# Optimization experiments

Hardware: AMD Instinct MI355X
Metric: run time of the kernel (lower is better)

## Reference

```python
import jax, jax.numpy as jnp
import numpy as np

B, S, D_MODEL, D_K = 4, 4096, 1024, 128
NEG = jnp.float32(-1e30)  # acts as -inf for masking; exp underflows to exactly 0 in fp32


def setup_inputs() -> dict:
    key = jax.random.key(0)
    ks = jax.random.split(key, 8)
    sc = 1.0 / np.sqrt(D_MODEL)
    x = jax.random.normal(ks[0], (B, S, D_MODEL), jnp.float32)
    padding_mask = (jax.random.uniform(ks[1], (B, S)) > 0.05).astype(jnp.float32)
    Wq = jax.random.normal(ks[2], (D_MODEL, D_K), jnp.float32) * sc
    bq = jax.random.normal(ks[3], (D_K,), jnp.float32) * 0.01
    Wk = jax.random.normal(ks[4], (D_MODEL, D_K), jnp.float32) * sc
    bk = jax.random.normal(ks[5], (D_K,), jnp.float32) * 0.01
    Wv = jax.random.normal(ks[6], (D_MODEL, D_K), jnp.float32) * sc
    bv = jax.random.normal(ks[7], (D_K,), jnp.float32) * 0.01
    return {"x": x, "padding_mask": padding_mask, "Wq": Wq, "bq": bq,
            "Wk": Wk, "bk": bk, "Wv": Wv, "bv": bv}


def reference(x, padding_mask, Wq, bq, Wk, bk, Wv, bv):
    # Self-attention path (enc_dec_layer_input is None), masked=True (causal).
    scale = jnp.sqrt(jnp.float32(Wq.shape[-1]))
    Q = x @ Wq + bq  # [B,S,Dk]
    K = x @ Wk + bk
    V = x @ Wv + bv
    scores = jnp.einsum('bqd,bkd->bqk', Q, K) / scale  # [B,S,S]
    # causal mask (torch: triu(1) filled with -inf) AND padding outer-product mask
    causal = jnp.tril(jnp.ones((S, S), dtype=bool))  # True = allowed
    pm = (padding_mask[:, :, None] * padding_mask[:, None, :]) > 0  # [B,S,S]
    allowed = causal[None] & pm
    scores = jnp.where(allowed, scores, NEG)
    attn = jax.nn.softmax(scores, axis=-1)
    # torch: fully-masked query rows give NaN -> nan_to_num -> 0.
    # A query row is dead iff its own token is padded (diagonal is causally allowed).
    row_alive = padding_mask > 0  # [B,S]
    attn = jnp.where(row_alive[:, :, None], attn, 0.0)
    out = jnp.einsum('bqk,bkd->bqd', attn, V)  # [B,S,Dk]
    return out
```

## Files before the change

kernel.cpp:

```cpp
#include <hip/hip_runtime.h>
#include <hip/hip_bf16.h>
#include <cstdint>

typedef __bf16 bf16x8 __attribute__((ext_vector_type(8)));
typedef float f32x4 __attribute__((ext_vector_type(4)));

#define MFMA16(a, b, c) __builtin_amdgcn_mfma_f32_16x16x32_bf16((a), (b), (c), 0, 0, 0)

__device__ __forceinline__ unsigned short f2bf(float f) {
  union { float f; unsigned u; } v; v.f = f;
  unsigned u = v.u;
  u += 0x7fffu + ((u >> 16) & 1u);
  return (unsigned short)(u >> 16);
}
__device__ __forceinline__ unsigned pk2(float a, float b) {
  __hip_bfloat162 h = __float22bfloat162_rn(make_float2(a, b));
  union { __hip_bfloat162 h; unsigned u; } v; v.h = h; return v.u;
}

__global__ __launch_bounds__(256) void convert_w(
    const float* __restrict__ Wq, const float* __restrict__ Wk,
    const float* __restrict__ Wv, unsigned short* __restrict__ wt) {
  int idx = blockIdx.x * 256 + threadIdx.x;
  int m = idx >> 17;
  int rem = idx & 131071;
  int k = rem >> 7;
  int n = rem & 127;
  const float* W = (m == 0) ? Wq : (m == 1) ? Wk : Wv;
  wt[(size_t)m * 131072 + (size_t)n * 1024 + k] = f2bf(W[(size_t)k * 128 + n]);
}

__global__ __launch_bounds__(256) void qkv_gemm(
    const float* __restrict__ x, const unsigned short* __restrict__ wt_all,
    const float* __restrict__ bq, const float* __restrict__ bk,
    const float* __restrict__ bv,
    unsigned short* __restrict__ Qg, unsigned short* __restrict__ Kg,
    unsigned short* __restrict__ Vtg) {
  __shared__ unsigned short x_lds[64][40];
  __shared__ unsigned short w_lds[128][40];
  const int tid = threadIdx.x;
  const int lane = tid & 63;
  const int w = tid >> 6;
  const int mode = blockIdx.y;
  const int m0 = blockIdx.x * 64;
  const unsigned short* wt = wt_all + (size_t)mode * 131072;
  const float* bias = (mode == 0) ? bq : (mode == 1) ? bk : bv;

  const int wr = (w >> 1) * 32;
  const int wc = (w & 1) * 64;
  const int lr = lane & 15;
  const int lk = (lane >> 4) * 8;

  f32x4 acc[2][4];
#pragma unroll
  for (int m = 0; m < 2; ++m)
#pragma unroll
    for (int n = 0; n < 4; ++n) acc[m][n] = (f32x4){0.f, 0.f, 0.f, 0.f};

  const int xr = tid >> 2;
  const int xc = (tid & 3) * 8;
  const int srow = tid >> 1;
  const int shalf = (tid & 1) * 16;
  const float* xrow = x + (size_t)(m0 + xr) * 1024 + xc;
  const unsigned short* wrow = wt + (size_t)srow * 1024 + shalf;

  float4 xa, xb; uint4 wv0, wv1;
  {
    const float4* s4 = (const float4*)xrow;
    xa = s4[0]; xb = s4[1];
    const uint4* ws4 = (const uint4*)wrow;
    wv0 = ws4[0]; wv1 = ws4[1];
  }

  for (int k0 = 0; k0 < 1024; k0 += 32) {
    __syncthreads();
    {
      uint4 xw;
      xw.x = pk2(xa.x, xa.y);  xw.y = pk2(xa.z, xa.w);
      xw.z = pk2(xb.x, xb.y);  xw.w = pk2(xb.z, xb.w);
      *(uint4*)&x_lds[xr][xc] = xw;
      *(uint4*)&w_lds[srow][shalf] = wv0;
      *(uint4*)&w_lds[srow][shalf + 8] = wv1;
    }
    __syncthreads();
    if (k0 + 32 < 1024) {
      const float4* s4 = (const float4*)(xrow + k0 + 32);
      xa = s4[0]; xb = s4[1];
      const uint4* ws4 = (const uint4*)(wrow + k0 + 32);
      wv0 = ws4[0]; wv1 = ws4[1];
    }
    bf16x8 af[2], bfr[4];
#pragma unroll
    for (int m = 0; m < 2; ++m) af[m] = *(const bf16x8*)&x_lds[wr + m * 16 + lr][lk];
#pragma unroll
    for (int n = 0; n < 4; ++n) bfr[n] = *(const bf16x8*)&w_lds[wc + n * 16 + lr][lk];
#pragma unroll
    for (int m = 0; m < 2; ++m)
#pragma unroll
      for (int n = 0; n < 4; ++n) acc[m][n] = MFMA16(af[m], bfr[n], acc[m][n]);
  }

  float bcol[4];
#pragma unroll
  for (int n = 0; n < 4; ++n) bcol[n] = bias[wc + n * 16 + lr];
#pragma unroll
  for (int m = 0; m < 2; ++m)
#pragma unroll
    for (int n = 0; n < 4; ++n)
#pragma unroll
      for (int r = 0; r < 4; ++r) {
        int grow = m0 + wr + m * 16 + (lane >> 4) * 4 + r;
        int col = wc + n * 16 + lr;
        float val = acc[m][n][r] + bcol[n];
        if (mode == 0) {
          val *= 0.08838834764831845f;
          Qg[(size_t)grow * 128 + col] = f2bf(val);
        } else if (mode == 1) {
          Kg[(size_t)grow * 128 + col] = f2bf(val);
        } else {
          int bb = grow >> 12, s = grow & 4095;
          Vtg[((size_t)bb * 128 + col) * 4096 + s] = f2bf(val);
        }
      }
}

struct AttnLds {
  union {
    unsigned short K_lds[64][136];
    unsigned short P_lds[4][16][68];
  } u;
  unsigned short V_lds[128][72];
};

__device__ __forceinline__ void attn_tiles(
    AttnLds& S, const unsigned short* __restrict__ Kb,
    const unsigned short* __restrict__ Vb, const float* __restrict__ pmb,
    int q0, int tstart, int tend,
    const bf16x8 (&qf)[4], float& mrow, float& lsum, f32x4 (&o)[8]) {
  const int tid = threadIdx.x;
  const int lane = tid & 63;
  const int w = tid >> 6;
  const int lr = lane & 15;
  const int lg = lane >> 4;
  const int lk = lg * 8;
  const int q_own = q0 + w * 16 + lr;

  for (int t = tstart; t < tend; ++t) {
    const int k0 = t * 64;
    __syncthreads();
    {
      int kr = tid >> 2, seg = (tid & 3) * 32;
      const uint4* src = (const uint4*)(Kb + (size_t)(k0 + kr) * 128 + seg);
      uint4 v0 = src[0], v1 = src[1], v2 = src[2], v3 = src[3];
      uint4* dst = (uint4*)&S.u.K_lds[kr][seg];
      dst[0] = v0; dst[1] = v1; dst[2] = v2; dst[3] = v3;
      int d = tid >> 1, half = (tid & 1) * 32;
      const uint4* vs = (const uint4*)(Vb + (size_t)d * 4096 + k0 + half);
      uint4 u0 = vs[0], u1 = vs[1], u2 = vs[2], u3 = vs[3];
      uint4* vdst = (uint4*)&S.V_lds[d][half];
      vdst[0] = u0; vdst[1] = u1; vdst[2] = u2; vdst[3] = u3;
    }
    __syncthreads();

    f32x4 st[4];
#pragma unroll
    for (int f = 0; f < 4; ++f) {
      st[f] = (f32x4){0.f, 0.f, 0.f, 0.f};
#pragma unroll
      for (int dc = 0; dc < 4; ++dc) {
        bf16x8 kf = *(const bf16x8*)&S.u.K_lds[f * 16 + lr][dc * 32 + lk];
        st[f] = MFMA16(kf, qf[dc], st[f]);
      }
    }

    const unsigned long long mb = __ballot(pmb[k0 + lane] > 0.f);
    unsigned nib[4];
#pragma unroll
    for (int f = 0; f < 4; ++f) nib[f] = (unsigned)(mb >> (16 * f + 4 * lg)) & 0xFu;

    __syncthreads();

    float mx = -1e30f;
    if (k0 + 63 > q0 + (w << 4)) {
#pragma unroll
      for (int f = 0; f < 4; ++f)
#pragma unroll
        for (int r = 0; r < 4; ++r) {
          const bool ok = (((nib[f] >> r) & 1u) != 0u) &&
                          (k0 + 16 * f + 4 * lg + r <= q_own);
          const float s = ok ? st[f][r] : -1e30f;
          st[f][r] = s;
          mx = fmaxf(mx, s);
        }
    } else {
#pragma unroll
      for (int f = 0; f < 4; ++f)
#pragma unroll
        for (int r = 0; r < 4; ++r) {
          const bool ok = ((nib[f] >> r) & 1u) != 0u;
          const float s = ok ? st[f][r] : -1e30f;
          st[f][r] = s;
          mx = fmaxf(mx, s);
        }
    }
    mx = fmaxf(mx, __shfl_xor(mx, 16));
    mx = fmaxf(mx, __shfl_xor(mx, 32));
    const float mnew = fmaxf(mrow, mx);
    const float alpha = __expf(mrow - mnew);
    mrow = mnew;

    float sum = 0.f;
#pragma unroll
    for (int f = 0; f < 4; ++f) {
      const float p0 = (st[f][0] < -1e29f) ? 0.f : __expf(st[f][0] - mnew);
      const float p1 = (st[f][1] < -1e29f) ? 0.f : __expf(st[f][1] - mnew);
      const float p2 = (st[f][2] < -1e29f) ? 0.f : __expf(st[f][2] - mnew);
      const float p3 = (st[f][3] < -1e29f) ? 0.f : __expf(st[f][3] - mnew);
      sum += (p0 + p1) + (p2 + p3);
      uint2 u; u.x = pk2(p0, p1); u.y = pk2(p2, p3);
      *(uint2*)&S.u.P_lds[w][lr][16 * f + 4 * lg] = u;
    }
    sum += __shfl_xor(sum, 16);
    sum += __shfl_xor(sum, 32);
    lsum = lsum * alpha + sum;
#pragma unroll
    for (int n = 0; n < 8; ++n) o[n] *= alpha;

    __asm__ volatile("s_waitcnt lgkmcnt(0)" ::: "memory");
#pragma unroll
    for (int kc = 0; kc < 2; ++kc) {
      bf16x8 pa = *(const bf16x8*)&S.u.P_lds[w][lr][kc * 32 + lk];
#pragma unroll
      for (int n = 0; n < 8; ++n) {
        bf16x8 vf = *(const bf16x8*)&S.V_lds[n * 16 + lr][kc * 32 + lk];
        o[n] = MFMA16(vf, pa, o[n]);
      }
    }
  }
}

__global__ __launch_bounds__(256, 4) void attn_fwd(
    const unsigned short* __restrict__ Qg, const unsigned short* __restrict__ Kg,
    const unsigned short* __restrict__ Vtg, const float* __restrict__ pmask,
    float* __restrict__ out) {
  __shared__ AttnLds S;
  const int tid = threadIdx.x;
  const int lane = tid & 63;
  const int w = tid >> 6;
  const int b = blockIdx.y;
  const int q0 = blockIdx.x * 64;
  const int lr = lane & 15;
  const int lg = lane >> 4;
  const int lk = lg * 8;

  bf16x8 qf[4];
  {
    const unsigned short* qp = Qg + ((size_t)b * 4096 + q0 + w * 16 + lr) * 128;
#pragma unroll
    for (int dc = 0; dc < 4; ++dc) qf[dc] = *(const bf16x8*)(qp + dc * 32 + lk);
  }
  float mrow = -1e30f, lsum = 0.f;
  f32x4 o[8];
#pragma unroll
  for (int n = 0; n < 8; ++n) o[n] = (f32x4){0.f, 0.f, 0.f, 0.f};

  attn_tiles(S, Kg + (size_t)b * 4096 * 128, Vtg + (size_t)b * 128 * 4096,
             pmask + (size_t)b * 4096, q0, 0, (q0 >> 6) + 1, qf, mrow, lsum, o);

  const int qrow = q0 + w * 16 + lr;
  const bool alive = pmask[(size_t)b * 4096 + qrow] > 0.f;
  const float inv = (alive && lsum > 0.f) ? 1.f / lsum : 0.f;
  float* op = out + ((size_t)b * 4096 + qrow) * 128 + 4 * lg;
#pragma unroll
  for (int n = 0; n < 8; ++n) {
    f32x4 v = o[n] * inv;
    *(f32x4*)(op + n * 16) = v;
  }
}

__global__ __launch_bounds__(256, 4) void attn_split(
    const unsigned short* __restrict__ Qg, const unsigned short* __restrict__ Kg,
    const unsigned short* __restrict__ Vtg, const float* __restrict__ pmask,
    float* __restrict__ out, unsigned short* __restrict__ o_part,
    float* __restrict__ ml_part) {
  __shared__ AttnLds S;
  const int tid = threadIdx.x;
  const int lane = tid & 63;
  const int w = tid >> 6;
  const int L = blockIdx.x;
  const int xcd = L & 7;
  const int b = xcd >> 1;
  const int s = ((L >> 3) << 1) | (xcd & 1);
  int qb, c, nch;
  if (s < 8) {
    qb = s; c = 0; nch = 1;
  } else {
    int g = 1;
#pragma unroll
    for (int gg = 2; gg <= 7; ++gg)
      if (s >= 4 * gg * (gg + 1)) g = gg;
    const int rel = s - 4 * g * (g + 1);
    const int qq = rel / (g + 1);
    qb = 8 * g + qq;
    c = rel - qq * (g + 1);
    nch = g + 1;
  }
  const int q0 = qb * 64;
  const int tstart = c * 8;
  const int tend = min(c * 8 + 8, qb + 1);
  const int lr = lane & 15;
  const int lg = lane >> 4;
  const int lk = lg * 8;

  bf16x8 qf[4];
  {
    const unsigned short* qp = Qg + ((size_t)b * 4096 + q0 + w * 16 + lr) * 128;
#pragma unroll
    for (int dc = 0; dc < 4; ++dc) qf[dc] = *(const bf16x8*)(qp + dc * 32 + lk);
  }
  float mrow = -1e30f, lsum = 0.f;
  f32x4 o[8];
#pragma unroll
  for (int n = 0; n < 8; ++n) o[n] = (f32x4){0.f, 0.f, 0.f, 0.f};

  attn_tiles(S, Kg + (size_t)b * 4096 * 128, Vtg + (size_t)b * 128 * 4096,
             pmask + (size_t)b * 4096, q0, tstart, tend, qf, mrow, lsum, o);

  if (nch == 1) {
    const int qrow = q0 + w * 16 + lr;
    const bool alive = pmask[(size_t)b * 4096 + qrow] > 0.f;
    const float inv = (alive && lsum > 0.f) ? 1.f / lsum : 0.f;
    float* op = out + ((size_t)b * 4096 + qrow) * 128 + 4 * lg;
#pragma unroll
    for (int n = 0; n < 8; ++n) {
      f32x4 v = o[n] * inv;
      *(f32x4*)(op + n * 16) = v;
    }
  } else {
    const int slot = b * 280 + (s - 8);
    unsigned short* op = o_part + ((size_t)slot * 64 + w * 16 + lr) * 128 + 4 * lg;
#pragma unroll
    for (int n = 0; n < 8; ++n) {
      uint2 u; u.x = pk2(o[n][0], o[n][1]); u.y = pk2(o[n][2], o[n][3]);
      *(uint2*)(op + n * 16) = u;
    }
    if (lane < 16) {
      float* mp = ml_part + ((size_t)slot * 64 + w * 16 + lane) * 2;
      mp[0] = mrow;
      mp[1] = lsum;
    }
  }
}

__global__ __launch_bounds__(256) void attn_combine(
    const unsigned short* __restrict__ o_part, const float* __restrict__ ml_part,
    const float* __restrict__ pmask, float* __restrict__ out) {
  const int tid = threadIdx.x;
  const int lane = tid & 63;
  const int w = tid >> 6;
  const int g = blockIdx.x * 4 + w;
  const int b = g / 3584;
  const int rem = g % 3584;
  const int qb = 8 + (rem >> 6);
  const int row = rem & 63;
  const int qrow = qb * 64 + row;
  const int grp = qb >> 3;
  const int nch = grp + 1;
  const int pbase = b * 280 + 4 * grp * (grp + 1) - 8 + (qb - 8 * grp) * nch;

  float m[8], l[8];
  float M = -1e30f;
#pragma unroll
  for (int c = 0; c < 8; ++c)
    if (c < nch) {
      const float* mp = ml_part + ((size_t)(pbase + c) * 64 + row) * 2;
      m[c] = mp[0];
      l[c] = mp[1];
      M = fmaxf(M, m[c]);
    }
  float L = 0.f, wgt[8];
#pragma unroll
  for (int c = 0; c < 8; ++c)
    if (c < nch) {
      wgt[c] = __expf(m[c] - M);
      L += wgt[c] * l[c];
    }
  float2 acc = {0.f, 0.f};
#pragma unroll
  for (int c = 0; c < 8; ++c)
    if (c < nch) {
      const unsigned u = *(const unsigned*)(o_part + ((size_t)(pbase + c) * 64 + row) * 128 + lane * 2);
      acc.x += wgt[c] * __uint_as_float(u << 16);
      acc.y += wgt[c] * __uint_as_float(u & 0xffff0000u);
    }
  const bool alive = pmask[(size_t)b * 4096 + qrow] > 0.f;
  const float inv = (alive && L > 0.f) ? 1.f / L : 0.f;
  float2* op = (float2*)(out + ((size_t)b * 4096 + qrow) * 128);
  op[lane] = make_float2(acc.x * inv, acc.y * inv);
}

extern "C" void kernel_launch(void* const* d_in, const int* in_sizes, int n_in,
                              void* d_out, int out_size, void* d_ws, size_t ws_size,
                              hipStream_t stream) {
  (void)in_sizes; (void)n_in; (void)out_size;
  const float* x  = (const float*)d_in[0];
  const float* pm = (const float*)d_in[1];
  const float* Wq = (const float*)d_in[2];
  const float* bq = (const float*)d_in[3];
  const float* Wk = (const float*)d_in[4];
  const float* bk = (const float*)d_in[5];
  const float* Wv = (const float*)d_in[6];
  const float* bv = (const float*)d_in[7];
  float* out = (float*)d_out;

  unsigned short* ws  = (unsigned short*)d_ws;
  unsigned short* wt  = ws;
  unsigned short* Qg  = ws + 393216;
  unsigned short* Kg  = Qg + 2097152;
  unsigned short* Vtg = Kg + 2097152;
  unsigned short* o_part = ws + 6684672;
  float* ml_part = (float*)(ws + 15859712);
  const size_t WS_NEED = 15859712u * 2u + 573440u;

  convert_w<<<1536, 256, 0, stream>>>(Wq, Wk, Wv, wt);
  qkv_gemm<<<dim3(256, 3), 256, 0, stream>>>(x, wt, bq, bk, bv, Qg, Kg, Vtg);
  if (ws_size >= WS_NEED) {
    attn_split<<<1152, 256, 0, stream>>>(Qg, Kg, Vtg, pm, out, o_part, ml_part);
    attn_combine<<<3584, 256, 0, stream>>>(o_part, ml_part, pm, out);
  } else {
    attn_fwd<<<dim3(64, 4), 256, 0, stream>>>(Qg, Kg, Vtg, pm, out);
  }
}
```

Before: 104.4 us.

## Fuse Q/K/V projections into one GEMM kernel sharing the x tile

Replaces the three-way grid split (one block per mode) with a single block computing Q, K and V for its 64-row slab. Each x tile is loaded from global and converted to bf16 once instead of three times. Global loads are double-buffered two k-steps ahead. In exchange, the grid shrinks from 768 to 256 blocks, each thread holds three times the accumulators, and more registers are live, which can lower occupancy and parallelism.

```diff
diff --git a/kernel.cpp b/kernel.cpp
--- a/kernel.cpp
+++ b/kernel.cpp
@@ -30,98 +30,138 @@
   wt[(size_t)m * 131072 + (size_t)n * 1024 + k] = f2bf(W[(size_t)k * 128 + n]);
 }
 
-__global__ __launch_bounds__(256) void qkv_gemm(
+__global__ __launch_bounds__(256) void qkv_fused(
     const float* __restrict__ x, const unsigned short* __restrict__ wt_all,
     const float* __restrict__ bq, const float* __restrict__ bk,
     const float* __restrict__ bv,
     unsigned short* __restrict__ Qg, unsigned short* __restrict__ Kg,
     unsigned short* __restrict__ Vtg) {
   __shared__ unsigned short x_lds[64][40];
-  __shared__ unsigned short w_lds[128][40];
+  __shared__ unsigned short w_lds[3][128][40];
   const int tid = threadIdx.x;
   const int lane = tid & 63;
   const int w = tid >> 6;
-  const int mode = blockIdx.y;
   const int m0 = blockIdx.x * 64;
-  const unsigned short* wt = wt_all + (size_t)mode * 131072;
-  const float* bias = (mode == 0) ? bq : (mode == 1) ? bk : bv;
-
   const int wr = (w >> 1) * 32;
   const int wc = (w & 1) * 64;
   const int lr = lane & 15;
   const int lk = (lane >> 4) * 8;
 
-  f32x4 acc[2][4];
-#pragma unroll
-  for (int m = 0; m < 2; ++m)
-#pragma unroll
-    for (int n = 0; n < 4; ++n) acc[m][n] = (f32x4){0.f, 0.f, 0.f, 0.f};
+  f32x4 acc[3][2][4];
+#pragma unroll
+  for (int md = 0; md < 3; ++md)
+#pragma unroll
+    for (int m = 0; m < 2; ++m)
+#pragma unroll
+      for (int n = 0; n < 4; ++n) acc[md][m][n] = (f32x4){0.f, 0.f, 0.f, 0.f};
 
   const int xr = tid >> 2;
   const int xc = (tid & 3) * 8;
   const int srow = tid >> 1;
   const int shalf = (tid & 1) * 16;
-  const float* xrow = x + (size_t)(m0 + xr) * 1024 + xc;
-  const unsigned short* wrow = wt + (size_t)srow * 1024 + shalf;
-
-  float4 xa, xb; uint4 wv0, wv1;
+  const float* xbase = x + (size_t)(m0 + xr) * 1024 + xc;
+  const unsigned short* w0p = wt_all + (size_t)srow * 1024 + shalf;
+  const unsigned short* w1p = w0p + 131072;
+  const unsigned short* w2p = w1p + 131072;
+
+  float4 xA0, xA1, xB0, xB1;
+  uint4 a0, a1, a2, a3, a4, a5, b0, b1, b2, b3, b4, b5;
   {
-    const float4* s4 = (const float4*)xrow;
-    xa = s4[0]; xb = s4[1];
-    const uint4* ws4 = (const uint4*)wrow;
-    wv0 = ws4[0]; wv1 = ws4[1];
-  }
-
-  for (int k0 = 0; k0 < 1024; k0 += 32) {
-    __syncthreads();
-    {
-      uint4 xw;
-      xw.x = pk2(xa.x, xa.y);  xw.y = pk2(xa.z, xa.w);
-      xw.z = pk2(xb.x, xb.y);  xw.w = pk2(xb.z, xb.w);
-      *(uint4*)&x_lds[xr][xc] = xw;
-      *(uint4*)&w_lds[srow][shalf] = wv0;
-      *(uint4*)&w_lds[srow][shalf + 8] = wv1;
-    }
-    __syncthreads();
-    if (k0 + 32 < 1024) {
-      const float4* s4 = (const float4*)(xrow + k0 + 32);
-      xa = s4[0]; xb = s4[1];
-      const uint4* ws4 = (const uint4*)(wrow + k0 + 32);
-      wv0 = ws4[0]; wv1 = ws4[1];
-    }
-    bf16x8 af[2], bfr[4];
-#pragma unroll
-    for (int m = 0; m < 2; ++m) af[m] = *(const bf16x8*)&x_lds[wr + m * 16 + lr][lk];
-#pragma unroll
-    for (int n = 0; n < 4; ++n) bfr[n] = *(const bf16x8*)&w_lds[wc + n * 16 + lr][lk];
+    const float4* p = (const float4*)xbase;
+    xA0 = p[0]; xA1 = p[1];
+    const uint4* q0 = (const uint4*)w0p; a0 = q0[0]; a1 = q0[1];
+    const uint4* q1 = (const uint4*)w1p; a2 = q1[0]; a3 = q1[1];
+    const uint4* q2 = (const uint4*)w2p; a4 = q2[0]; a5 = q2[1];
+  }
+  {
+    const float4* p = (const float4*)(xbase + 32);
+    xB0 = p[0]; xB1 = p[1];
+    const uint4* q0 = (const uint4*)(w0p + 32); b0 = q0[0]; b1 = q0[1];
+    const uint4* q1 = (const uint4*)(w1p + 32); b2 = q1[0]; b3 = q1[1];
+    const uint4* q2 = (const uint4*)(w2p + 32); b4 = q2[0]; b5 = q2[1];
+  }
+
+#define QKV_STORE(X0, X1, W0, W1, W2, W3, W4, W5)             \
+  {                                                            \
+    uint4 xw;                                                  \
+    xw.x = pk2(X0.x, X0.y); xw.y = pk2(X0.z, X0.w);            \
+    xw.z = pk2(X1.x, X1.y); xw.w = pk2(X1.z, X1.w);            \
+    *(uint4*)&x_lds[xr][xc] = xw;                              \
+    *(uint4*)&w_lds[0][srow][shalf] = W0;                      \
+    *(uint4*)&w_lds[0][srow][shalf + 8] = W1;                  \
+    *(uint4*)&w_lds[1][srow][shalf] = W2;                      \
+    *(uint4*)&w_lds[1][srow][shalf + 8] = W3;                  \
+    *(uint4*)&w_lds[2][srow][shalf] = W4;                      \
+    *(uint4*)&w_lds[2][srow][shalf + 8] = W5;                  \
+  }
+
+#define QKV_COMPUTE()                                          \
+  {                                                            \
+    bf16x8 af0 = *(const bf16x8*)&x_lds[wr + lr][lk];          \
+    bf16x8 af1 = *(const bf16x8*)&x_lds[wr + 16 + lr][lk];     \
+    _Pragma("unroll")                                          \
+    for (int md = 0; md < 3; ++md)                             \
+      _Pragma("unroll")                                        \
+      for (int n = 0; n < 4; ++n) {                            \
+        bf16x8 bfv = *(const bf16x8*)&w_lds[md][wc + n * 16 + lr][lk]; \
+        acc[md][0][n] = MFMA16(af0, bfv, acc[md][0][n]);       \
+        acc[md][1][n] = MFMA16(af1, bfv, acc[md][1][n]);       \
+      }                                                        \
+  }
+
+  for (int k0 = 0; k0 < 1024; k0 += 64) {
+    __syncthreads();
+    QKV_STORE(xA0, xA1, a0, a1, a2, a3, a4, a5);
+    __syncthreads();
+    if (k0 + 64 < 1024) {
+      const float4* p = (const float4*)(xbase + k0 + 64);
+      xA0 = p[0]; xA1 = p[1];
+      const uint4* q0 = (const uint4*)(w0p + k0 + 64); a0 = q0[0]; a1 = q0[1];
+      const uint4* q1 = (const uint4*)(w1p + k0 + 64); a2 = q1[0]; a3 = q1[1];
+      const uint4* q2 = (const uint4*)(w2p + k0 + 64); a4 = q2[0]; a5 = q2[1];
+    }
+    QKV_COMPUTE();
+    __syncthreads();
+    QKV_STORE(xB0, xB1, b0, b1, b2, b3, b4, b5);
+    __syncthreads();
+    if (k0 + 96 < 1024) {
+      const float4* p = (const float4*)(xbase + k0 + 96);
+      xB0 = p[0]; xB1 = p[1];
+      const uint4* q0 = (const uint4*)(w0p + k0 + 96); b0 = q0[0]; b1 = q0[1];
+      const uint4* q1 = (const uint4*)(w1p + k0 + 96); b2 = q1[0]; b3 = q1[1];
+      const uint4* q2 = (const uint4*)(w2p + k0 + 96); b4 = q2[0]; b5 = q2[1];
+    }
+    QKV_COMPUTE();
+  }
+#undef QKV_STORE
+#undef QKV_COMPUTE
+
+#pragma unroll
+  for (int md = 0; md < 3; ++md) {
+    const float* bias = (md == 0) ? bq : (md == 1) ? bk : bv;
+    float bcol[4];
+#pragma unroll
+    for (int n = 0; n < 4; ++n) bcol[n] = bias[wc + n * 16 + lr];
 #pragma unroll
     for (int m = 0; m < 2; ++m)
 #pragma unroll
-      for (int n = 0; n < 4; ++n) acc[m][n] = MFMA16(af[m], bfr[n], acc[m][n]);
-  }
-
-  float bcol[4];
-#pragma unroll
-  for (int n = 0; n < 4; ++n) bcol[n] = bias[wc + n * 16 + lr];
-#pragma unroll
-  for (int m = 0; m < 2; ++m)
-#pragma unroll
-    for (int n = 0; n < 4; ++n)
-#pragma unroll
-      for (int r = 0; r < 4; ++r) {
-        int grow = m0 + wr + m * 16 + (lane >> 4) * 4 + r;
-        int col = wc + n * 16 + lr;
-        float val = acc[m][n][r] + bcol[n];
-        if (mode == 0) {
-          val *= 0.08838834764831845f;
-          Qg[(size_t)grow * 128 + col] = f2bf(val);
-        } else if (mode == 1) {
-          Kg[(size_t)grow * 128 + col] = f2bf(val);
-        } else {
-          int bb = grow >> 12, s = grow & 4095;
-          Vtg[((size_t)bb * 128 + col) * 4096 + s] = f2bf(val);
+      for (int n = 0; n < 4; ++n)
+#pragma unroll
+        for (int r = 0; r < 4; ++r) {
+          int grow = m0 + wr + m * 16 + (lane >> 4) * 4 + r;
+          int col = wc + n * 16 + lr;
+          float val = acc[md][m][n][r] + bcol[n];
+          if (md == 0) {
+            val *= 0.08838834764831845f;
+            Qg[(size_t)grow * 128 + col] = f2bf(val);
+          } else if (md == 1) {
+            Kg[(size_t)grow * 128 + col] = f2bf(val);
+          } else {
+            int bb = grow >> 12, s = grow & 4095;
+            Vtg[((size_t)bb * 128 + col) * 4096 + s] = f2bf(val);
+          }
         }
-      }
+  }
 }
 
 struct AttnLds {
@@ -423,7 +463,7 @@
   const size_t WS_NEED = 15859712u * 2u + 573440u;
 
   convert_w<<<1536, 256, 0, stream>>>(Wq, Wk, Wv, wt);
-  qkv_gemm<<<dim3(256, 3), 256, 0, stream>>>(x, wt, bq, bk, bv, Qg, Kg, Vtg);
+  qkv_fused<<<256, 256, 0, stream>>>(x, wt, bq, bk, bv, Qg, Kg, Vtg);
   if (ws_size >= WS_NEED) {
     attn_split<<<1152, 256, 0, stream>>>(Qg, Kg, Vtg, pm, out, o_part, ml_part);
     attn_combine<<<3584, 256, 0, stream>>>(o_part, ml_part, pm, out);
```

Result: slower. 107.6 us (+3.1%).

## Fuse Q/K/V projections into one GEMM block sharing each x tile

Applied to the files above, without the earlier changes.

Replaces the three-way grid split (one block per Q, K or V) with a single 512-thread block that computes all 384 output columns for a 64-row tile of x. Each x tile is loaded and converted to bf16 once instead of three times, cutting global reads of the fp32 input roughly threefold. Loads are double-buffered in registers two k-steps deep. The cost is fewer blocks (256 instead of 768), a larger LDS weight tile, and more registers per thread, which may lower occupancy.

```diff
diff --git a/kernel.cpp b/kernel.cpp
--- a/kernel.cpp
+++ b/kernel.cpp
@@ -30,98 +30,119 @@
   wt[(size_t)m * 131072 + (size_t)n * 1024 + k] = f2bf(W[(size_t)k * 128 + n]);
 }
 
-__global__ __launch_bounds__(256) void qkv_gemm(
+__global__ __launch_bounds__(512) void qkv_fused(
     const float* __restrict__ x, const unsigned short* __restrict__ wt_all,
     const float* __restrict__ bq, const float* __restrict__ bk,
     const float* __restrict__ bv,
     unsigned short* __restrict__ Qg, unsigned short* __restrict__ Kg,
     unsigned short* __restrict__ Vtg) {
   __shared__ unsigned short x_lds[64][40];
-  __shared__ unsigned short w_lds[128][40];
+  __shared__ unsigned short w_lds[384][40];
   const int tid = threadIdx.x;
   const int lane = tid & 63;
   const int w = tid >> 6;
-  const int mode = blockIdx.y;
   const int m0 = blockIdx.x * 64;
-  const unsigned short* wt = wt_all + (size_t)mode * 131072;
-  const float* bias = (mode == 0) ? bq : (mode == 1) ? bk : bv;
-
-  const int wr = (w >> 1) * 32;
-  const int wc = (w & 1) * 64;
+  const int rh = w >> 2;
+  const int cq = w & 3;
   const int lr = lane & 15;
   const int lk = (lane >> 4) * 8;
 
-  f32x4 acc[2][4];
+  f32x4 acc[2][6];
 #pragma unroll
   for (int m = 0; m < 2; ++m)
 #pragma unroll
-    for (int n = 0; n < 4; ++n) acc[m][n] = (f32x4){0.f, 0.f, 0.f, 0.f};
-
-  const int xr = tid >> 2;
-  const int xc = (tid & 3) * 8;
-  const int srow = tid >> 1;
-  const int shalf = (tid & 1) * 16;
-  const float* xrow = x + (size_t)(m0 + xr) * 1024 + xc;
-  const unsigned short* wrow = wt + (size_t)srow * 1024 + shalf;
-
-  float4 xa, xb; uint4 wv0, wv1;
+    for (int n = 0; n < 6; ++n) acc[m][n] = (f32x4){0.f, 0.f, 0.f, 0.f};
+
+  const int xr = tid >> 3;
+  const int xc = (tid & 7) * 4;
+  const float* xbase = x + (size_t)(m0 + xr) * 1024 + xc;
+  const int j0 = tid, j1 = tid + 512, j2 = tid + 1024;
+  const int wr0 = j0 >> 2, ws0 = (j0 & 3) * 8;
+  const int wr1 = j1 >> 2, ws1 = (j1 & 3) * 8;
+  const int wr2 = j2 >> 2, ws2 = (j2 & 3) * 8;
+  const unsigned short* wp0 = wt_all + (size_t)wr0 * 1024 + ws0;
+  const unsigned short* wp1 = wt_all + (size_t)wr1 * 1024 + ws1;
+  const unsigned short* wp2 = wt_all + (size_t)wr2 * 1024 + ws2;
+
+  float4 xA, xB;
+  uint4 wA0, wA1, wA2, wB0, wB1, wB2;
   {
-    const float4* s4 = (const float4*)xrow;
-    xa = s4[0]; xb = s4[1];
-    const uint4* ws4 = (const uint4*)wrow;
-    wv0 = ws4[0]; wv1 = ws4[1];
-  }
-
-  for (int k0 = 0; k0 < 1024; k0 += 32) {
-    __syncthreads();
-    {
-      uint4 xw;
-      xw.x = pk2(xa.x, xa.y);  xw.y = pk2(xa.z, xa.w);
-      xw.z = pk2(xb.x, xb.y);  xw.w = pk2(xb.z, xb.w);
-      *(uint4*)&x_lds[xr][xc] = xw;
-      *(uint4*)&w_lds[srow][shalf] = wv0;
-      *(uint4*)&w_lds[srow][shalf + 8] = wv1;
-    }
-    __syncthreads();
-    if (k0 + 32 < 1024) {
-      const float4* s4 = (const float4*)(xrow + k0 + 32);
-      xa = s4[0]; xb = s4[1];
-      const uint4* ws4 = (const uint4*)(wrow + k0 + 32);
-      wv0 = ws4[0]; wv1 = ws4[1];
-    }
-    bf16x8 af[2], bfr[4];
-#pragma unroll
-    for (int m = 0; m < 2; ++m) af[m] = *(const bf16x8*)&x_lds[wr + m * 16 + lr][lk];
-#pragma unroll
-    for (int n = 0; n < 4; ++n) bfr[n] = *(const bf16x8*)&w_lds[wc + n * 16 + lr][lk];
+    xA = *(const float4*)xbase;
+    wA0 = *(const uint4*)wp0; wA1 = *(const uint4*)wp1; wA2 = *(const uint4*)wp2;
+    xB = *(const float4*)(xbase + 32);
+    wB0 = *(const uint4*)(wp0 + 32); wB1 = *(const uint4*)(wp1 + 32); wB2 = *(const uint4*)(wp2 + 32);
+  }
+
+#define QKV_STORE(X, W0, W1, W2)                               \
+  {                                                            \
+    uint2 xw;                                                  \
+    xw.x = pk2(X.x, X.y); xw.y = pk2(X.z, X.w);                \
+    *(uint2*)&x_lds[xr][xc] = xw;                              \
+    *(uint4*)&w_lds[wr0][ws0] = W0;                            \
+    *(uint4*)&w_lds[wr1][ws1] = W1;                            \
+    *(uint4*)&w_lds[wr2][ws2] = W2;                            \
+  }
+
+#define QKV_COMPUTE()                                          \
+  {                                                            \
+    bf16x8 af0 = *(const bf16x8*)&x_lds[rh * 32 + lr][lk];     \
+    bf16x8 af1 = *(const bf16x8*)&x_lds[rh * 32 + 16 + lr][lk];\
+    _Pragma("unroll")                                          \
+    for (int n = 0; n < 6; ++n) {                              \
+      bf16x8 bfv = *(const bf16x8*)&w_lds[cq * 96 + n * 16 + lr][lk]; \
+      acc[0][n] = MFMA16(af0, bfv, acc[0][n]);                 \
+      acc[1][n] = MFMA16(af1, bfv, acc[1][n]);                 \
+    }                                                          \
+  }
+
+  for (int k0 = 0; k0 < 1024; k0 += 64) {
+    __syncthreads();
+    QKV_STORE(xA, wA0, wA1, wA2);
+    __syncthreads();
+    if (k0 + 64 < 1024) {
+      xA = *(const float4*)(xbase + k0 + 64);
+      wA0 = *(const uint4*)(wp0 + k0 + 64);
+      wA1 = *(const uint4*)(wp1 + k0 + 64);
+      wA2 = *(const uint4*)(wp2 + k0 + 64);
+    }
+    QKV_COMPUTE();
+    __syncthreads();
+    QKV_STORE(xB, wB0, wB1, wB2);
+    __syncthreads();
+    if (k0 + 96 < 1024) {
+      xB = *(const float4*)(xbase + k0 + 96);
+      wB0 = *(const uint4*)(wp0 + k0 + 96);
+      wB1 = *(const uint4*)(wp1 + k0 + 96);
+      wB2 = *(const uint4*)(wp2 + k0 + 96);
+    }
+    QKV_COMPUTE();
+  }
+#undef QKV_STORE
+#undef QKV_COMPUTE
+
+#pragma unroll
+  for (int n = 0; n < 6; ++n) {
+    const int gcol = cq * 96 + n * 16 + lr;
+    const int mode = gcol >> 7;
+    const int col = gcol & 127;
+    const float bias = (mode == 0) ? bq[col] : (mode == 1) ? bk[col] : bv[col];
 #pragma unroll
     for (int m = 0; m < 2; ++m)
 #pragma unroll
-      for (int n = 0; n < 4; ++n) acc[m][n] = MFMA16(af[m], bfr[n], acc[m][n]);
-  }
-
-  float bcol[4];
-#pragma unroll
-  for (int n = 0; n < 4; ++n) bcol[n] = bias[wc + n * 16 + lr];
-#pragma unroll
-  for (int m = 0; m < 2; ++m)
-#pragma unroll
-    for (int n = 0; n < 4; ++n)
-#pragma unroll
       for (int r = 0; r < 4; ++r) {
-        int grow = m0 + wr + m * 16 + (lane >> 4) * 4 + r;
-        int col = wc + n * 16 + lr;
-        float val = acc[m][n][r] + bcol[n];
+        const int grow = m0 + rh * 32 + m * 16 + (lane >> 4) * 4 + r;
+        float val = acc[m][n][r] + bias;
         if (mode == 0) {
           val *= 0.08838834764831845f;
           Qg[(size_t)grow * 128 + col] = f2bf(val);
         } else if (mode == 1) {
           Kg[(size_t)grow * 128 + col] = f2bf(val);
         } else {
-          int bb = grow >> 12, s = grow & 4095;
+          const int bb = grow >> 12, s = grow & 4095;
           Vtg[((size_t)bb * 128 + col) * 4096 + s] = f2bf(val);
         }
       }
+  }
 }
 
 struct AttnLds {
@@ -423,7 +444,7 @@
   const size_t WS_NEED = 15859712u * 2u + 573440u;
 
   convert_w<<<1536, 256, 0, stream>>>(Wq, Wk, Wv, wt);
-  qkv_gemm<<<dim3(256, 3), 256, 0, stream>>>(x, wt, bq, bk, bv, Qg, Kg, Vtg);
+  qkv_fused<<<256, 512, 0, stream>>>(x, wt, bq, bk, bv, Qg, Kg, Vtg);
   if (ws_size >= WS_NEED) {
     attn_split<<<1152, 256, 0, stream>>>(Qg, Kg, Vtg, pm, out, o_part, ml_part);
     attn_combine<<<3584, 256, 0, stream>>>(o_part, ml_part, pm, out);
```

Measured after the change: 106.9 us. 2.4% more time.

## Double attention query tile to 128 rows with 512-thread blocks

Applied to the files above, without the earlier changes.

Attention blocks now handle 128 query rows with 8 waves (512 threads), so each K/V tile loaded into LDS is reused by twice as many queries. The split-KV schedule, partial-slot indexing and combine indexing are rewritten for 128-row query blocks, and cooperative loads are redistributed across 512 threads. This cuts global K/V traffic per query and the number of partials to combine. In exchange there is more causal-diagonal waste per block, fewer blocks in flight, and an occupancy hint (launch bounds 512, 8) that may squeeze registers.

```diff
diff --git a/kernel.cpp b/kernel.cpp
--- a/kernel.cpp
+++ b/kernel.cpp
@@ -127,7 +127,7 @@
 struct AttnLds {
   union {
     unsigned short K_lds[64][136];
-    unsigned short P_lds[4][16][68];
+    unsigned short P_lds[8][16][68];
   } u;
   unsigned short V_lds[128][72];
 };
@@ -145,20 +145,21 @@
   const int lk = lg * 8;
   const int q_own = q0 + w * 16 + lr;
 
+  const int kr = tid >> 3, kseg = (tid & 7) * 16;
+  const int vd = tid >> 2, vseg = (tid & 3) * 16;
+
   for (int t = tstart; t < tend; ++t) {
     const int k0 = t * 64;
     __syncthreads();
     {
-      int kr = tid >> 2, seg = (tid & 3) * 32;
-      const uint4* src = (const uint4*)(Kb + (size_t)(k0 + kr) * 128 + seg);
-      uint4 v0 = src[0], v1 = src[1], v2 = src[2], v3 = src[3];
-      uint4* dst = (uint4*)&S.u.K_lds[kr][seg];
-      dst[0] = v0; dst[1] = v1; dst[2] = v2; dst[3] = v3;
-      int d = tid >> 1, half = (tid & 1) * 32;
-      const uint4* vs = (const uint4*)(Vb + (size_t)d * 4096 + k0 + half);
-      uint4 u0 = vs[0], u1 = vs[1], u2 = vs[2], u3 = vs[3];
-      uint4* vdst = (uint4*)&S.V_lds[d][half];
-      vdst[0] = u0; vdst[1] = u1; vdst[2] = u2; vdst[3] = u3;
+      const uint4* ks = (const uint4*)(Kb + (size_t)(k0 + kr) * 128 + kseg);
+      uint4 ka = ks[0], kb = ks[1];
+      uint4* kd = (uint4*)&S.u.K_lds[kr][kseg];
+      kd[0] = ka; kd[1] = kb;
+      const uint4* vs = (const uint4*)(Vb + (size_t)vd * 4096 + k0 + vseg);
+      uint4 va = vs[0], vb = vs[1];
+      uint4* vdst = (uint4*)&S.V_lds[vd][vseg];
+      vdst[0] = va; vdst[1] = vb;
     }
     __syncthreads();
 
@@ -239,7 +240,7 @@
   }
 }
 
-__global__ __launch_bounds__(256, 4) void attn_fwd(
+__global__ __launch_bounds__(512, 8) void attn_fwd(
     const unsigned short* __restrict__ Qg, const unsigned short* __restrict__ Kg,
     const unsigned short* __restrict__ Vtg, const float* __restrict__ pmask,
     float* __restrict__ out) {
@@ -248,7 +249,7 @@
   const int lane = tid & 63;
   const int w = tid >> 6;
   const int b = blockIdx.y;
-  const int q0 = blockIdx.x * 64;
+  const int q0 = blockIdx.x * 128;
   const int lr = lane & 15;
   const int lg = lane >> 4;
   const int lk = lg * 8;
@@ -265,7 +266,7 @@
   for (int n = 0; n < 8; ++n) o[n] = (f32x4){0.f, 0.f, 0.f, 0.f};
 
   attn_tiles(S, Kg + (size_t)b * 4096 * 128, Vtg + (size_t)b * 128 * 4096,
-             pmask + (size_t)b * 4096, q0, 0, (q0 >> 6) + 1, qf, mrow, lsum, o);
+             pmask + (size_t)b * 4096, q0, 0, (q0 >> 6) + 2, qf, mrow, lsum, o);
 
   const int qrow = q0 + w * 16 + lr;
   const bool alive = pmask[(size_t)b * 4096 + qrow] > 0.f;
@@ -278,7 +279,7 @@
   }
 }
 
-__global__ __launch_bounds__(256, 4) void attn_split(
+__global__ __launch_bounds__(512, 8) void attn_split(
     const unsigned short* __restrict__ Qg, const unsigned short* __restrict__ Kg,
     const unsigned short* __restrict__ Vtg, const float* __restrict__ pmask,
     float* __restrict__ out, unsigned short* __restrict__ o_part,
@@ -291,23 +292,23 @@
   const int xcd = L & 7;
   const int b = xcd >> 1;
   const int s = ((L >> 3) << 1) | (xcd & 1);
-  int qb, c, nch;
-  if (s < 8) {
-    qb = s; c = 0; nch = 1;
+  int qb2, c, nch;
+  if (s < 4) {
+    qb2 = s; c = 0; nch = 1;
   } else {
-    int g = 1;
-#pragma unroll
-    for (int gg = 2; gg <= 7; ++gg)
-      if (s >= 4 * gg * (gg + 1)) g = gg;
-    const int rel = s - 4 * g * (g + 1);
-    const int qq = rel / (g + 1);
-    qb = 8 * g + qq;
-    c = rel - qq * (g + 1);
-    nch = g + 1;
-  }
-  const int q0 = qb * 64;
+    int n = 2;
+#pragma unroll
+    for (int nn = 3; nn <= 8; ++nn)
+      if (s >= 2 * nn * (nn - 1)) n = nn;
+    const int rel = s - 2 * n * (n - 1);
+    const int qq = rel / n;
+    qb2 = 4 * (n - 1) + qq;
+    c = rel - qq * n;
+    nch = n;
+  }
+  const int q0 = qb2 * 128;
   const int tstart = c * 8;
-  const int tend = min(c * 8 + 8, qb + 1);
+  const int tend = min(c * 8 + 8, 2 * qb2 + 2);
   const int lr = lane & 15;
   const int lg = lane >> 4;
   const int lk = lg * 8;
@@ -337,15 +338,16 @@
       *(f32x4*)(op + n * 16) = v;
     }
   } else {
-    const int slot = b * 280 + (s - 8);
-    unsigned short* op = o_part + ((size_t)slot * 64 + w * 16 + lr) * 128 + 4 * lg;
+    const int slot = b * 140 + 2 * nch * (nch - 1) - 4 + (qb2 - 4 * (nch - 1)) * nch + c;
+    const int row = w * 16 + lr;
+    unsigned short* op = o_part + ((size_t)slot * 128 + row) * 128 + 4 * lg;
 #pragma unroll
     for (int n = 0; n < 8; ++n) {
       uint2 u; u.x = pk2(o[n][0], o[n][1]); u.y = pk2(o[n][2], o[n][3]);
       *(uint2*)(op + n * 16) = u;
     }
     if (lane < 16) {
-      float* mp = ml_part + ((size_t)slot * 64 + w * 16 + lane) * 2;
+      float* mp = ml_part + ((size_t)slot * 128 + w * 16 + lane) * 2;
       mp[0] = mrow;
       mp[1] = lsum;
     }
@@ -361,19 +363,18 @@
   const int g = blockIdx.x * 4 + w;
   const int b = g / 3584;
   const int rem = g % 3584;
-  const int qb = 8 + (rem >> 6);
-  const int row = rem & 63;
-  const int qrow = qb * 64 + row;
-  const int grp = qb >> 3;
-  const int nch = grp + 1;
-  const int pbase = b * 280 + 4 * grp * (grp + 1) - 8 + (qb - 8 * grp) * nch;
+  const int qb2 = 4 + (rem >> 7);
+  const int row = rem & 127;
+  const int qrow = qb2 * 128 + row;
+  const int nch = (2 * qb2 + 9) >> 3;
+  const int pbase = b * 140 + 2 * nch * (nch - 1) - 4 + (qb2 - 4 * (nch - 1)) * nch;
 
   float m[8], l[8];
   float M = -1e30f;
 #pragma unroll
   for (int c = 0; c < 8; ++c)
     if (c < nch) {
-      const float* mp = ml_part + ((size_t)(pbase + c) * 64 + row) * 2;
+      const float* mp = ml_part + ((size_t)(pbase + c) * 128 + row) * 2;
       m[c] = mp[0];
       l[c] = mp[1];
       M = fmaxf(M, m[c]);
@@ -389,7 +390,7 @@
 #pragma unroll
   for (int c = 0; c < 8; ++c)
     if (c < nch) {
-      const unsigned u = *(const unsigned*)(o_part + ((size_t)(pbase + c) * 64 + row) * 128 + lane * 2);
+      const unsigned u = *(const unsigned*)(o_part + ((size_t)(pbase + c) * 128 + row) * 128 + lane * 2);
       acc.x += wgt[c] * __uint_as_float(u << 16);
       acc.y += wgt[c] * __uint_as_float(u & 0xffff0000u);
     }
@@ -425,9 +426,9 @@
   convert_w<<<1536, 256, 0, stream>>>(Wq, Wk, Wv, wt);
   qkv_gemm<<<dim3(256, 3), 256, 0, stream>>>(x, wt, bq, bk, bv, Qg, Kg, Vtg);
   if (ws_size >= WS_NEED) {
-    attn_split<<<1152, 256, 0, stream>>>(Qg, Kg, Vtg, pm, out, o_part, ml_part);
+    attn_split<<<576, 512, 0, stream>>>(Qg, Kg, Vtg, pm, out, o_part, ml_part);
     attn_combine<<<3584, 256, 0, stream>>>(o_part, ml_part, pm, out);
   } else {
-    attn_fwd<<<dim3(64, 4), 256, 0, stream>>>(Qg, Kg, Vtg, pm, out);
-  }
-}
+    attn_fwd<<<dim3(32, 4), 512, 0, stream>>>(Qg, Kg, Vtg, pm, out);
+  }
+}
```

New measurement: 178.9 us. 71.4% more time.
